# Kernel optimization log

Hardware: AMD Instinct MI355X
Metric: run time of the kernel (lower is better)

The kernel has to match this reference:

```python
import jax, jax.numpy as jnp
import numpy as np

A = 9
C = 80
TOPK = 1000            # topk_candidates
NMS_THRESH = 0.5
SCORE_THRESH = 0.05
DET_PER_IMG = 100      # detections_per_img
BBOX_XFORM_CLIP = float(np.log(1000.0 / 16.0))
CLASS_OFFSET = 4096.0  # > any clipped coordinate -> class-aware NMS trick


def setup_inputs() -> dict:
    key = jax.random.key(0)
    ks = jax.random.split(key, 4)
    B = 8
    levels = [(128, 128, 4096, 8), (64, 64, 2048, 16), (32, 32, 1024, 32)]  # H, W, K, stride
    inp = {}
    for i, (H, W, K, stride) in enumerate(levels):
        k1, k2, k3, k4, k5, k6, k7, k8 = jax.random.split(ks[i], 8)
        # plausible anchor boxes (x1, y1, x2, y2) with positive width/height
        cx = jax.random.uniform(k1, (B, H, W, A)) * (W * stride)
        cy = jax.random.uniform(k2, (B, H, W, A)) * (H * stride)
        w = 16.0 + jax.random.uniform(k3, (B, H, W, A)) * 112.0
        h = 16.0 + jax.random.uniform(k4, (B, H, W, A)) * 112.0
        anch = jnp.stack([cx - 0.5 * w, cy - 0.5 * h, cx + 0.5 * w, cy + 0.5 * h], axis=-1)
        # [B, H, W, A, 4] -> [B, 4A, H, W] (A groups of 4 along channel, matching permute(1,2,0) + reshape(-1,4))
        inp[f"anchors_{i}"] = jnp.transpose(anch.reshape(B, H, W, 4 * A), (0, 3, 1, 2)).astype(jnp.float32)
        coords = jnp.stack(
            [jax.random.randint(k5, (B, K), 0, H), jax.random.randint(k6, (B, K), 0, W)], axis=-1
        ).astype(jnp.int32)
        inp[f"coords_{i}"] = coords
        inp[f"score_logits_{i}"] = (jax.random.normal(k7, (B, K, A * C)) * 2.0 - 2.0).astype(jnp.float32)
        inp[f"regs_{i}"] = (jax.random.normal(k8, (B, K, A * 4)) * 0.2).astype(jnp.float32)
    inp["image_shapes"] = jnp.full((B, 2), 1024.0, dtype=jnp.float32)  # (h, w) per image
    return inp


def _decode(boxes, deltas, img_hw):
    # boxes, deltas: [N, 4] (x1, y1, x2, y2) / (dx, dy, dw, dh)
    x1, y1, x2, y2 = boxes[:, 0], boxes[:, 1], boxes[:, 2], boxes[:, 3]
    w = x2 - x1
    h = y2 - y1
    cx = x1 + 0.5 * w
    cy = y1 + 0.5 * h
    dx, dy = deltas[:, 0], deltas[:, 1]
    dw = jnp.minimum(deltas[:, 2], BBOX_XFORM_CLIP)
    dh = jnp.minimum(deltas[:, 3], BBOX_XFORM_CLIP)
    pcx = dx * w + cx
    pcy = dy * h + cy
    pw = jnp.exp(dw) * w
    ph = jnp.exp(dh) * h
    ih, iw = img_hw[0], img_hw[1]
    nx1 = jnp.clip(pcx - 0.5 * pw, 0.0, iw)
    ny1 = jnp.clip(pcy - 0.5 * ph, 0.0, ih)
    nx2 = jnp.clip(pcx + 0.5 * pw, 0.0, iw)
    ny2 = jnp.clip(pcy + 0.5 * ph, 0.0, ih)
    return jnp.stack([nx1, ny1, nx2, ny2], axis=-1)


def _level(anchor_map, coords, logits, regs, img_hw):
    # anchor_map: [4A, H, W]; coords: [K, 2]; logits: [K, A*C]; regs: [K, A*4]
    bb = jnp.transpose(anchor_map, (1, 2, 0))[coords[:, 0], coords[:, 1]]  # [K, 4A]
    boxes = bb.reshape(-1, 4)            # [K*A, 4]
    deltas = regs.reshape(-1, 4)         # [K*A, 4]
    dec = _decode(boxes, deltas, img_hw)
    scores = jax.nn.sigmoid(logits.reshape(-1, C))  # [K*A, C]
    flat = scores.reshape(-1)                       # [K*A*C]
    k = min(TOPK, flat.shape[0])
    top_s, idx = jax.lax.top_k(flat, k)
    return dec[idx // C], top_s, (idx % C)


def _pairwise_iou(b):
    area = (b[:, 2] - b[:, 0]) * (b[:, 3] - b[:, 1])
    lt = jnp.maximum(b[:, None, :2], b[None, :, :2])
    rb = jnp.minimum(b[:, None, 2:], b[None, :, 2:])
    wh = jnp.clip(rb - lt, 0.0)
    inter = wh[..., 0] * wh[..., 1]
    return inter / (area[:, None] + area[None, :] - inter + 1e-9)


def _nms(boxes, scores, labels):
    # class-aware NMS with fixed-size output [DET_PER_IMG, 6]
    order = jnp.argsort(-scores)
    b = boxes[order]
    s = scores[order]
    l = labels[order]
    iou = _pairwise_iou(b + l.astype(b.dtype)[:, None] * CLASS_OFFSET)  # [N, N]
    N = s.shape[0]
    idxs = jnp.arange(N)
    valid = s > SCORE_THRESH

    def body(i, keep):
        sup = (iou[i] > NMS_THRESH) & (idxs > i) & keep[i]
        return keep & ~sup

    keep = jax.lax.fori_loop(0, N, body, valid)
    masked = jnp.where(keep, s, -1.0)
    top_s, top_i = jax.lax.top_k(masked, DET_PER_IMG)
    pad = top_s > 0.0
    out_b = jnp.where(pad[:, None], b[top_i], 0.0)
    out_l = jnp.where(pad, l[top_i], -1).astype(b.dtype)
    return jnp.concatenate([out_b, top_s[:, None], out_l[:, None]], axis=-1)  # [DET, 6]


def _per_image(a0, a1, a2, c0, c1, c2, s0, s1, s2, r0, r1, r2, hw):
    parts = [
        _level(a, c, sl, r, hw)
        for a, c, sl, r in zip((a0, a1, a2), (c0, c1, c2), (s0, s1, s2), (r0, r1, r2))
    ]
    boxes = jnp.concatenate([p[0] for p in parts], axis=0)
    scores = jnp.concatenate([p[1] for p in parts], axis=0)
    labels = jnp.concatenate([p[2] for p in parts], axis=0)
    return _nms(boxes, scores, labels)


def reference(anchors_0, anchors_1, anchors_2, coords_0, coords_1, coords_2,
              score_logits_0, score_logits_1, score_logits_2,
              regs_0, regs_1, regs_2, image_shapes):
    # returns [B, DET_PER_IMG, 6] = (x1, y1, x2, y2, score, label); padded rows have score -1, label -1
    return jax.vmap(_per_image)(
        anchors_0, anchors_1, anchors_2,
        coords_0, coords_1, coords_2,
        score_logits_0, score_logits_1, score_logits_2,
        regs_0, regs_1, regs_2, image_shapes,
    )
```

## Files before the change

### kernel.cpp

```cpp
#include <hip/hip_runtime.h>

typedef unsigned long long u64;
typedef unsigned int u32;

#define NIMG 8
#define NLVL 3
#define TOPKN 1000
#define NC3 3000
#define DETS 100
#define PRETH 3.0f
#define NBINS 3072
#define LCAP 2048
#define MROWS 256
#define NW 47
#define NWP 48
#define CAP 32768
#define GPAD 16

#define NBLK0 5760
#define NBLK1 2880
#define NBLK2 1440
#define NBLKTOT 10080

__device__ __forceinline__ u32 fmap(float f) {
  u32 b = __float_as_uint(f);
  return (b & 0x80000000u) ? ~b : (b | 0x80000000u);
}
__device__ __forceinline__ float funmap(u32 u) {
  u32 b = (u & 0x80000000u) ? (u & 0x7FFFFFFFu) : ~u;
  return __uint_as_float(b);
}

__global__ __launch_bounds__(256) void k_prefilter(
    const float* __restrict__ lg0, const float* __restrict__ lg1,
    const float* __restrict__ lg2, u64* __restrict__ dense,
    u32* __restrict__ gcnt) {
  __shared__ int s_wcnt[4];
  __shared__ u32 s_base;
  const int tid = threadIdx.x, wave = tid >> 6, lane = tid & 63;
  int blk = blockIdx.x;
  const float* lg; int imgElems, lblk, lvl;
  if (blk < NBLK0)              { lg = lg0; imgElems = 2949120; lblk = blk; lvl = 0; }
  else if (blk < NBLK0 + NBLK1) { lg = lg1; imgElems = 1474560; lblk = blk - NBLK0; lvl = 1; }
  else                          { lg = lg2; imgElems = 737280;  lblk = blk - NBLK0 - NBLK1; lvl = 2; }
  int ce = lblk * 4096 + wave * 1024;
  int img = ce / imgElems;
  int flatBase = ce - img * imgElems;
  const float* src = lg + (size_t)img * imgElems;
  const int dst = img * NLVL + lvl;
  u64 lmask = (1ull << lane) - 1ull;
  float va[16];
#pragma unroll
  for (int r = 0; r < 4; ++r) {
    const float4 v = *(const float4*)(src + flatBase + r * 256 + lane * 4);
    va[r * 4 + 0] = v.x; va[r * 4 + 1] = v.y;
    va[r * 4 + 2] = v.z; va[r * 4 + 3] = v.w;
  }
  int total = 0;
#pragma unroll
  for (int u = 0; u < 16; ++u) total += __popcll(__ballot(va[u] > PRETH));
  if (lane == 0) s_wcnt[wave] = total;
  __syncthreads();
  if (tid == 0) {
    u32 bt = (u32)(s_wcnt[0] + s_wcnt[1] + s_wcnt[2] + s_wcnt[3]);
    s_base = bt ? atomicAdd(&gcnt[dst * GPAD], bt) : 0u;
  }
  __syncthreads();
  u32 base = s_base;
  for (int w2 = 0; w2 < wave; ++w2) base += (u32)s_wcnt[w2];
  u64* db = dense + (size_t)dst * CAP;
  int off = 0;
#pragma unroll
  for (int u = 0; u < 16; ++u) {
    bool p = va[u] > PRETH;
    u64 m = __ballot(p);
    if (p) {
      int idx = flatBase + (u >> 2) * 256 + lane * 4 + (u & 3);
      u32 fm = fmap(va[u]);
      u32 pos = base + (u32)(off + __popcll(m & lmask));
      if (pos < CAP) db[pos] = ((u64)fm << 32) | (u64)(~(u32)idx);
    }
    off += __popcll(m);
  }
}

__global__ __launch_bounds__(1024) void k_select(
    const u64* __restrict__ dense, const u32* __restrict__ gcnt,
    u64* __restrict__ topk) {
  __shared__ u32 hist[NBINS];
  __shared__ u64 lk[LCAP];
  __shared__ u32 wsum[16], wpre[16];
  __shared__ int sT, sM;
  const int bi = blockIdx.x;
  const int tid = threadIdx.x, wave = tid >> 6, lane = tid & 63;

  const u64 SAFE = ((u64)0x3E5FFFFFu << 32) | 0xFFFFFFFFull;
  if (tid < TOPKN) topk[(size_t)bi * TOPKN + tid] = SAFE;
  for (int i = tid; i < NBINS; i += 1024) hist[i] = 0;
  if (tid == 0) { sM = 0; sT = 0; }
  __syncthreads();

  u32 N = gcnt[bi * GPAD]; if (N > CAP) N = CAP;
  const u64* src = dense + (size_t)bi * CAP;
  for (u32 i = tid; i < N; i += 1024) {
    u32 bin = ((u32)(src[i] >> 32) - 0xC0000000u) >> 13;
    if (bin > NBINS - 1) bin = NBINS - 1;
    atomicAdd(&hist[bin], 1u);
  }
  __syncthreads();

  const int h0 = NBINS - 1 - tid * 3;
  u32 a0 = hist[h0], a1 = hist[h0 - 1], a2 = hist[h0 - 2];
  u32 s = a0 + a1 + a2;
  u32 inc = s;
#pragma unroll
  for (int d = 1; d < 64; d <<= 1) {
    u32 t = (u32)__shfl_up((int)inc, d);
    if (lane >= d) inc += t;
  }
  if (lane == 63) wsum[wave] = inc;
  __syncthreads();
  if (tid < 16) {
    u32 w = wsum[tid];
    u32 wi = w;
#pragma unroll
    for (int d = 1; d < 16; d <<= 1) {
      u32 t = (u32)__shfl_up((int)wi, d);
      if (tid >= d) wi += t;
    }
    wpre[tid] = wi - w;
  }
  __syncthreads();
  u32 excl = wpre[wave] + (inc - s);
  if (excl < TOPKN && excl + s >= TOPKN) {
    u32 acc = excl + a0;
    int T;
    if (acc >= TOPKN) T = h0;
    else { acc += a1; T = (acc >= TOPKN) ? h0 - 1 : h0 - 2; }
    sT = T;
  }
  __syncthreads();
  const int T = sT;

  for (u32 i = tid; i < N; i += 1024) {
    u64 key = src[i];
    u32 bin = ((u32)(key >> 32) - 0xC0000000u) >> 13;
    if (bin > NBINS - 1) bin = NBINS - 1;
    if ((int)bin >= T) {
      int q = atomicAdd(&sM, 1);
      if (q < LCAP) lk[q] = key;
    }
  }
  __syncthreads();
  int M = sM; if (M > LCAP) M = LCAP;
  u64 k0 = 0, k1 = 0;
  const bool have0 = tid < M, have1 = tid + 1024 < M;
  if (have0) k0 = lk[tid];
  if (have1) k1 = lk[tid + 1024];
  int r0 = 0, r1 = 0;
  for (int j = 0; j < M; ++j) {
    u64 kj = lk[j];
    r0 += (kj > k0);
    r1 += (kj > k1);
  }
  if (have0 && r0 < TOPKN) topk[(size_t)bi * TOPKN + r0] = k0;
  if (have1 && r1 < TOPKN) topk[(size_t)bi * TOPKN + r1] = k1;
}

__global__ __launch_bounds__(1024) void k_build(
    const u64* __restrict__ topk,
    const float* __restrict__ an0, const float* __restrict__ an1, const float* __restrict__ an2,
    const int* __restrict__ co0, const int* __restrict__ co1, const int* __restrict__ co2,
    const float* __restrict__ rg0, const float* __restrict__ rg1, const float* __restrict__ rg2,
    const float* __restrict__ ishape,
    float4* __restrict__ sbox, float* __restrict__ sscore, int* __restrict__ slabel) {
  __shared__ u64 keys[NC3];
  const int b = blockIdx.x, tid = threadIdx.x;
  const double ih = (double)ishape[b * 2 + 0];
  const double iw = (double)ishape[b * 2 + 1];
  const double CLIPV = 4.1351665567423563;
  float4 mb[3]; float ms[3]; int ml[3]; u64 mk[3]; bool mv[3];
  for (int q = 0; q < 3; ++q) {
    int c = tid + q * 1024;
    mv[q] = (c < NC3);
    mk[q] = 0ull;
    if (!mv[q]) continue;
    int l = c / 1000, pos = c - l * 1000;
    u64 key = topk[(size_t)(b * NLVL + l) * TOPKN + pos];
    u32 hi = (u32)(key >> 32);
    u32 flat = ~((u32)key);
    float logit = funmap(hi);
    int cls = (int)(flat % 80u);
    int bidx = (int)(flat / 80u);
    int k = bidx / 9, a = bidx - k * 9;
    const float* an; const int* co; const float* rg; int K, H, W;
    if (l == 0)      { an = an0; co = co0; rg = rg0; K = 4096; H = 128; W = 128; }
    else if (l == 1) { an = an1; co = co1; rg = rg1; K = 2048; H = 64;  W = 64;  }
    else             { an = an2; co = co2; rg = rg2; K = 1024; H = 32;  W = 32;  }
    if (k >= K) k = K - 1;
    int y = co[(b * K + k) * 2 + 0], x = co[(b * K + k) * 2 + 1];
    int HW = H * W;
    const float* ap = an + (size_t)(b * 36 + a * 4) * HW + y * W + x;
    double x1 = (double)ap[0], y1 = (double)ap[HW];
    double x2 = (double)ap[2 * HW], y2 = (double)ap[3 * HW];
    const float* rp = rg + (size_t)(b * K + k) * 36 + a * 4;
    double dx = (double)rp[0], dy = (double)rp[1];
    double dw = fmin((double)rp[2], CLIPV), dh = fmin((double)rp[3], CLIPV);
    double w = x2 - x1, h = y2 - y1;
    double cx = x1 + 0.5 * w, cy = y1 + 0.5 * h;
    double pcx = dx * w + cx, pcy = dy * h + cy;
    double pw = exp(dw) * w, ph = exp(dh) * h;
    double nx1 = fmin(fmax(pcx - 0.5 * pw, 0.0), iw);
    double ny1 = fmin(fmax(pcy - 0.5 * ph, 0.0), ih);
    double nx2 = fmin(fmax(pcx + 0.5 * pw, 0.0), iw);
    double ny2 = fmin(fmax(pcy + 0.5 * ph, 0.0), ih);
    mb[q] = make_float4((float)nx1, (float)ny1, (float)nx2, (float)ny2);
    ms[q] = (float)(1.0 / (1.0 + exp(-(double)logit)));
    ml[q] = cls;
    mk[q] = ((u64)hi << 32) | (u64)(~(u32)c);
    keys[c] = mk[q];
  }
  __syncthreads();
  for (int q = 0; q < 3; ++q) {
    if (!mv[q]) continue;
    int c = tid + q * 1024;
    int l = c / 1000, pos = c - l * 1000;
    int rank = pos;
    u64 key = mk[q];
#pragma unroll
    for (int m = 0; m < 3; ++m) {
      if (m == l) continue;
      int lo = 0, hi2 = 1000, base = m * 1000;
      while (lo < hi2) {
        int mid = (lo + hi2) >> 1;
        if (keys[base + mid] > key) lo = mid + 1; else hi2 = mid;
      }
      rank += lo;
    }
    sbox[(size_t)b * NC3 + rank] = mb[q];
    sscore[(size_t)b * NC3 + rank] = ms[q];
    slabel[(size_t)b * NC3 + rank] = ml[q];
  }
}

__global__ __launch_bounds__(256) void k_mask(
    const float4* __restrict__ sbox, const int* __restrict__ slabel,
    u64* __restrict__ mask) {
  __shared__ float4 qb[NC3];
  __shared__ float ar[NC3];
  const int img = blockIdx.x >> 4;
  const int r0 = (blockIdx.x & 15) * 16;
  const int tid = threadIdx.x, wave = tid >> 6, lane = tid & 63;
  for (int i = tid; i < NC3; i += 256) {
    float4 bx = sbox[(size_t)img * NC3 + i];
    float off = (float)slabel[(size_t)img * NC3 + i] * 4096.0f;
    float4 q = make_float4(bx.x + off, bx.y + off, bx.z + off, bx.w + off);
    qb[i] = q;
    ar[i] = (q.z - q.x) * (q.w - q.y);
  }
  __syncthreads();
  u64* mbase = mask + (size_t)img * MROWS * NWP;
  for (int q = 0; q < 4; ++q) {
    int i = r0 + wave * 4 + q;
    float4 bi = qb[i];
    float ai = ar[i];
    for (int w = 0; w < NW; ++w) {
      int j = w * 64 + lane;
      bool pred = false;
      if (j > i && j < NC3) {
        float4 bj = qb[j];
        float ltx = fmaxf(bi.x, bj.x), lty = fmaxf(bi.y, bj.y);
        float rbx = fminf(bi.z, bj.z), rby = fminf(bi.w, bj.w);
        float wx = fmaxf(rbx - ltx, 0.f), wy = fmaxf(rby - lty, 0.f);
        float inter = wx * wy;
        float denom = ((ai + ar[j]) - inter) + 1e-9f;
        pred = (inter / denom) > 0.5f;
      }
      u64 m = __ballot(pred);
      if (lane == 0) mbase[(size_t)i * NWP + w] = m;
    }
  }
}

__global__ __launch_bounds__(64) void k_serial(
    const float4* __restrict__ sbox, const float* __restrict__ sscore,
    const int* __restrict__ slabel, const u64* __restrict__ mask,
    float* __restrict__ out) {
  __shared__ int keptIdx[DETS];
  const int img = blockIdx.x, lane = threadIdx.x;
  const float* sc = sscore + (size_t)img * NC3;
  u64 mykeep = 0;
  for (int w = 0; w < NW; ++w) {
    int j = w * 64 + lane;
    float s = (j < NC3) ? sc[j] : -1.f;
    u64 m = __ballot(s > 0.05f);
    if (lane == w) mykeep = m;
  }
  const u64* mbase = mask + (size_t)img * MROWS * NWP;
  u64 pend[4];
  for (int d = 0; d < 4; ++d)
    pend[d] = (lane < NW) ? mbase[(size_t)d * NWP + lane] : 0ull;
  int cnt = 0;
  for (int i = 0; i < NC3; ++i) {
    u64 row = pend[i & 3];
    int nxt = i + 4;
    if (nxt < MROWS) pend[i & 3] = (lane < NW) ? mbase[(size_t)nxt * NWP + lane] : 0ull;
    int w = i >> 6;
    u64 kw = __shfl(mykeep, w);
    if ((kw >> (i & 63)) & 1ull) {
      if (lane == 0) keptIdx[cnt] = i;
      cnt++;
      if (cnt == DETS) break;
      if (i < MROWS) {
        mykeep &= ~row;
      } else {
        float4 bx = sbox[(size_t)img * NC3 + i];
        float off = (float)slabel[(size_t)img * NC3 + i] * 4096.0f;
        float bix = bx.x + off, biy = bx.y + off;
        float biz = bx.z + off, biw = bx.w + off;
        float ai = (biz - bix) * (biw - biy);
        for (int w2 = 0; w2 < NW; ++w2) {
          int j = w2 * 64 + lane;
          bool pred = false;
          if (j > i && j < NC3) {
            float4 bj = sbox[(size_t)img * NC3 + j];
            float o2 = (float)slabel[(size_t)img * NC3 + j] * 4096.0f;
            float jx = bj.x + o2, jy = bj.y + o2;
            float jz = bj.z + o2, jw = bj.w + o2;
            float aj = (jz - jx) * (jw - jy);
            float ltx = fmaxf(bix, jx), lty = fmaxf(biy, jy);
            float rbx = fminf(biz, jz), rby = fminf(biw, jw);
            float wx = fmaxf(rbx - ltx, 0.f), wy = fmaxf(rby - lty, 0.f);
            float inter = wx * wy;
            float denom = ((ai + aj) - inter) + 1e-9f;
            pred = (inter / denom) > 0.5f;
          }
          u64 m = __ballot(pred);
          if (lane == w2) mykeep &= ~m;
        }
      }
    }
  }
  __syncthreads();
  for (int s = lane; s < DETS; s += 64) {
    float* o = out + ((size_t)img * DETS + s) * 6;
    if (s < cnt) {
      int i = keptIdx[s];
      float4 bx = sbox[(size_t)img * NC3 + i];
      o[0] = bx.x; o[1] = bx.y; o[2] = bx.z; o[3] = bx.w;
      o[4] = sc[i];
      o[5] = (float)slabel[(size_t)img * NC3 + i];
    } else {
      o[0] = 0.f; o[1] = 0.f; o[2] = 0.f; o[3] = 0.f;
      o[4] = -1.0f; o[5] = -1.0f;
    }
  }
}

extern "C" void kernel_launch(void* const* d_in, const int* in_sizes, int n_in,
                              void* d_out, int out_size, void* d_ws, size_t ws_size,
                              hipStream_t stream) {
  int ia0, ic0, is0, ir0, ia1, ic1, is1, ir1, ia2, ic2, is2, ir2, ihw;
  if (in_sizes[1] == 8 * 4096 * 2) {
    ia0 = 0; ic0 = 1; is0 = 2; ir0 = 3;
    ia1 = 4; ic1 = 5; is1 = 6; ir1 = 7;
    ia2 = 8; ic2 = 9; is2 = 10; ir2 = 11; ihw = 12;
  } else {
    ia0 = 0; ia1 = 1; ia2 = 2;
    ic0 = 3; ic1 = 4; ic2 = 5;
    is0 = 6; is1 = 7; is2 = 8;
    ir0 = 9; ir1 = 10; ir2 = 11; ihw = 12;
  }

  u32* gcnt = (u32*)d_ws;
  u64* dense = (u64*)((char*)d_ws + 2048);
  u64* topk = dense + (size_t)NIMG * NLVL * CAP;
  float4* sboxp = (float4*)(topk + NIMG * NLVL * TOPKN);
  float* sscore = (float*)(sboxp + NIMG * NC3);
  int* slabel = (int*)(sscore + NIMG * NC3);
  u64* maskp = (u64*)(slabel + NIMG * NC3);
  float* out = (float*)d_out;

  hipMemsetAsync(d_ws, 0, 2048, stream);

  k_prefilter<<<NBLKTOT, 256, 0, stream>>>(
      (const float*)d_in[is0], (const float*)d_in[is1], (const float*)d_in[is2],
      dense, gcnt);
  k_select<<<NIMG * NLVL, 1024, 0, stream>>>(dense, gcnt, topk);
  k_build<<<NIMG, 1024, 0, stream>>>(topk,
      (const float*)d_in[ia0], (const float*)d_in[ia1], (const float*)d_in[ia2],
      (const int*)d_in[ic0], (const int*)d_in[ic1], (const int*)d_in[ic2],
      (const float*)d_in[ir0], (const float*)d_in[ir1], (const float*)d_in[ir2],
      (const float*)d_in[ihw],
      sboxp, sscore, slabel);
  k_mask<<<NIMG * 16, 256, 0, stream>>>(sboxp, slabel, maskp);
  k_serial<<<NIMG, 64, 0, stream>>>(sboxp, sscore, slabel, maskp, out);
}
```

Before: 415.5 us.

## Shard prefilter atomic counters per wave and stage NMS mask rows in LDS

The prefilter now has each wave reserve output slots with its own atomic on one of 32 sub-bucket counters per image-level. This removes the two block-wide barriers and the single hot atomic per image-level. k_select walks the 32 sub-buckets per wave instead of one dense list. Separately, k_serial runs with 256 threads to cooperatively stage the first 128 mask rows and all scores into LDS before the single-wave serial NMS loop. The risks are per-sub-bucket overflow (1536 slots each, which could drop candidates under skewed inputs) and a larger memset.

```diff
diff --git a/kernel.cpp b/kernel.cpp
--- a/kernel.cpp
+++ b/kernel.cpp
@@ -12,9 +12,11 @@
 #define NBINS 3072
 #define LCAP 2048
 #define MROWS 256
+#define MLDS 128
 #define NW 47
 #define NWP 48
-#define CAP 32768
+#define NSUB 32
+#define SUBCAP 1536
 #define GPAD 16
 
 #define NBLK0 5760
@@ -35,8 +37,6 @@
     const float* __restrict__ lg0, const float* __restrict__ lg1,
     const float* __restrict__ lg2, u64* __restrict__ dense,
     u32* __restrict__ gcnt) {
-  __shared__ int s_wcnt[4];
-  __shared__ u32 s_base;
   const int tid = threadIdx.x, wave = tid >> 6, lane = tid & 63;
   int blk = blockIdx.x;
   const float* lg; int imgElems, lblk, lvl;
@@ -48,6 +48,7 @@
   int flatBase = ce - img * imgElems;
   const float* src = lg + (size_t)img * imgElems;
   const int dst = img * NLVL + lvl;
+  const int sub = (lblk * 4 + wave) & (NSUB - 1);
   u64 lmask = (1ull << lane) - 1ull;
   float va[16];
 #pragma unroll
@@ -56,29 +57,26 @@
     va[r * 4 + 0] = v.x; va[r * 4 + 1] = v.y;
     va[r * 4 + 2] = v.z; va[r * 4 + 3] = v.w;
   }
+  u64 bm[16];
   int total = 0;
 #pragma unroll
-  for (int u = 0; u < 16; ++u) total += __popcll(__ballot(va[u] > PRETH));
-  if (lane == 0) s_wcnt[wave] = total;
-  __syncthreads();
-  if (tid == 0) {
-    u32 bt = (u32)(s_wcnt[0] + s_wcnt[1] + s_wcnt[2] + s_wcnt[3]);
-    s_base = bt ? atomicAdd(&gcnt[dst * GPAD], bt) : 0u;
-  }
-  __syncthreads();
-  u32 base = s_base;
-  for (int w2 = 0; w2 < wave; ++w2) base += (u32)s_wcnt[w2];
-  u64* db = dense + (size_t)dst * CAP;
+  for (int u = 0; u < 16; ++u) {
+    bm[u] = __ballot(va[u] > PRETH);
+    total += __popcll(bm[u]);
+  }
+  u32 base = 0;
+  if (lane == 0 && total)
+    base = atomicAdd(&gcnt[(dst * NSUB + sub) * GPAD], (u32)total);
+  base = (u32)__shfl((int)base, 0);
+  u64* db = dense + ((size_t)dst * NSUB + sub) * SUBCAP;
   int off = 0;
 #pragma unroll
   for (int u = 0; u < 16; ++u) {
-    bool p = va[u] > PRETH;
-    u64 m = __ballot(p);
-    if (p) {
+    u64 m = bm[u];
+    if ((m >> lane) & 1ull) {
       int idx = flatBase + (u >> 2) * 256 + lane * 4 + (u & 3);
-      u32 fm = fmap(va[u]);
       u32 pos = base + (u32)(off + __popcll(m & lmask));
-      if (pos < CAP) db[pos] = ((u64)fm << 32) | (u64)(~(u32)idx);
+      if (pos < SUBCAP) db[pos] = ((u64)fmap(va[u]) << 32) | (u64)(~(u32)idx);
     }
     off += __popcll(m);
   }
@@ -90,6 +88,7 @@
   __shared__ u32 hist[NBINS];
   __shared__ u64 lk[LCAP];
   __shared__ u32 wsum[16], wpre[16];
+  __shared__ u32 scnt[NSUB];
   __shared__ int sT, sM;
   const int bi = blockIdx.x;
   const int tid = threadIdx.x, wave = tid >> 6, lane = tid & 63;
@@ -97,15 +96,22 @@
   const u64 SAFE = ((u64)0x3E5FFFFFu << 32) | 0xFFFFFFFFull;
   if (tid < TOPKN) topk[(size_t)bi * TOPKN + tid] = SAFE;
   for (int i = tid; i < NBINS; i += 1024) hist[i] = 0;
+  if (tid < NSUB) {
+    u32 c = gcnt[(bi * NSUB + tid) * GPAD];
+    scnt[tid] = c > SUBCAP ? SUBCAP : c;
+  }
   if (tid == 0) { sM = 0; sT = 0; }
   __syncthreads();
 
-  u32 N = gcnt[bi * GPAD]; if (N > CAP) N = CAP;
-  const u64* src = dense + (size_t)bi * CAP;
-  for (u32 i = tid; i < N; i += 1024) {
-    u32 bin = ((u32)(src[i] >> 32) - 0xC0000000u) >> 13;
-    if (bin > NBINS - 1) bin = NBINS - 1;
-    atomicAdd(&hist[bin], 1u);
+  const u64* src = dense + (size_t)bi * NSUB * SUBCAP;
+  for (int s = wave; s < NSUB; s += 16) {
+    u32 c = scnt[s];
+    const u64* sp = src + (size_t)s * SUBCAP;
+    for (u32 i = lane; i < c; i += 64) {
+      u32 bin = ((u32)(sp[i] >> 32) - 0xC0000000u) >> 13;
+      if (bin > NBINS - 1) bin = NBINS - 1;
+      atomicAdd(&hist[bin], 1u);
+    }
   }
   __syncthreads();
 
@@ -142,13 +148,17 @@
   __syncthreads();
   const int T = sT;
 
-  for (u32 i = tid; i < N; i += 1024) {
-    u64 key = src[i];
-    u32 bin = ((u32)(key >> 32) - 0xC0000000u) >> 13;
-    if (bin > NBINS - 1) bin = NBINS - 1;
-    if ((int)bin >= T) {
-      int q = atomicAdd(&sM, 1);
-      if (q < LCAP) lk[q] = key;
+  for (int s2 = wave; s2 < NSUB; s2 += 16) {
+    u32 c = scnt[s2];
+    const u64* sp = src + (size_t)s2 * SUBCAP;
+    for (u32 i = lane; i < c; i += 64) {
+      u64 key = sp[i];
+      u32 bin = ((u32)(key >> 32) - 0xC0000000u) >> 13;
+      if (bin > NBINS - 1) bin = NBINS - 1;
+      if ((int)bin >= T) {
+        int q = atomicAdd(&sM, 1);
+        if (q < LCAP) lk[q] = key;
+      }
     }
   }
   __syncthreads();
@@ -282,73 +292,87 @@
   }
 }
 
-__global__ __launch_bounds__(64) void k_serial(
+__global__ __launch_bounds__(256) void k_serial(
     const float4* __restrict__ sbox, const float* __restrict__ sscore,
     const int* __restrict__ slabel, const u64* __restrict__ mask,
     float* __restrict__ out) {
+  __shared__ u64 sm_mask[MLDS * NWP];
+  __shared__ float sm_sc[NC3];
   __shared__ int keptIdx[DETS];
-  const int img = blockIdx.x, lane = threadIdx.x;
+  __shared__ int s_cnt;
+  const int img = blockIdx.x, tid = threadIdx.x, wave = tid >> 6, lane = tid & 63;
+  const u64* mbase = mask + (size_t)img * MROWS * NWP;
   const float* sc = sscore + (size_t)img * NC3;
-  u64 mykeep = 0;
-  for (int w = 0; w < NW; ++w) {
-    int j = w * 64 + lane;
-    float s = (j < NC3) ? sc[j] : -1.f;
-    u64 m = __ballot(s > 0.05f);
-    if (lane == w) mykeep = m;
-  }
-  const u64* mbase = mask + (size_t)img * MROWS * NWP;
-  u64 pend[4];
-  for (int d = 0; d < 4; ++d)
-    pend[d] = (lane < NW) ? mbase[(size_t)d * NWP + lane] : 0ull;
-  int cnt = 0;
-  for (int i = 0; i < NC3; ++i) {
-    u64 row = pend[i & 3];
-    int nxt = i + 4;
-    if (nxt < MROWS) pend[i & 3] = (lane < NW) ? mbase[(size_t)nxt * NWP + lane] : 0ull;
-    int w = i >> 6;
-    u64 kw = __shfl(mykeep, w);
-    if ((kw >> (i & 63)) & 1ull) {
-      if (lane == 0) keptIdx[cnt] = i;
-      cnt++;
-      if (cnt == DETS) break;
-      if (i < MROWS) {
-        mykeep &= ~row;
-      } else {
-        float4 bx = sbox[(size_t)img * NC3 + i];
-        float off = (float)slabel[(size_t)img * NC3 + i] * 4096.0f;
-        float bix = bx.x + off, biy = bx.y + off;
-        float biz = bx.z + off, biw = bx.w + off;
-        float ai = (biz - bix) * (biw - biy);
-        for (int w2 = 0; w2 < NW; ++w2) {
-          int j = w2 * 64 + lane;
-          bool pred = false;
-          if (j > i && j < NC3) {
-            float4 bj = sbox[(size_t)img * NC3 + j];
-            float o2 = (float)slabel[(size_t)img * NC3 + j] * 4096.0f;
-            float jx = bj.x + o2, jy = bj.y + o2;
-            float jz = bj.z + o2, jw = bj.w + o2;
-            float aj = (jz - jx) * (jw - jy);
-            float ltx = fmaxf(bix, jx), lty = fmaxf(biy, jy);
-            float rbx = fminf(biz, jz), rby = fminf(biw, jw);
-            float wx = fmaxf(rbx - ltx, 0.f), wy = fmaxf(rby - lty, 0.f);
-            float inter = wx * wy;
-            float denom = ((ai + aj) - inter) + 1e-9f;
-            pred = (inter / denom) > 0.5f;
+  for (int i = tid; i < MLDS * NWP; i += 256) sm_mask[i] = mbase[i];
+  for (int i = tid; i < NC3; i += 256) sm_sc[i] = sc[i];
+  __syncthreads();
+  if (wave == 0) {
+    u64 mykeep = 0;
+    for (int w = 0; w < NW; ++w) {
+      int j = w * 64 + lane;
+      float s = (j < NC3) ? sm_sc[j] : -1.f;
+      u64 m = __ballot(s > 0.05f);
+      if (lane == w) mykeep = m;
+    }
+    u64 pend[4];
+    for (int d = 0; d < 4; ++d)
+      pend[d] = (lane < NW) ? sm_mask[d * NWP + lane] : 0ull;
+    int cnt = 0;
+    for (int i = 0; i < NC3; ++i) {
+      u64 row = pend[i & 3];
+      int nxt = i + 4;
+      if (nxt < MROWS)
+        pend[i & 3] = (lane < NW)
+            ? ((nxt < MLDS) ? sm_mask[nxt * NWP + lane]
+                            : mbase[(size_t)nxt * NWP + lane])
+            : 0ull;
+      int w = i >> 6;
+      u64 kw = __shfl(mykeep, w);
+      if ((kw >> (i & 63)) & 1ull) {
+        if (lane == 0) keptIdx[cnt] = i;
+        cnt++;
+        if (cnt == DETS) break;
+        if (i < MROWS) {
+          mykeep &= ~row;
+        } else {
+          float4 bx = sbox[(size_t)img * NC3 + i];
+          float off = (float)slabel[(size_t)img * NC3 + i] * 4096.0f;
+          float bix = bx.x + off, biy = bx.y + off;
+          float biz = bx.z + off, biw = bx.w + off;
+          float ai = (biz - bix) * (biw - biy);
+          for (int w2 = 0; w2 < NW; ++w2) {
+            int j = w2 * 64 + lane;
+            bool pred = false;
+            if (j > i && j < NC3) {
+              float4 bj = sbox[(size_t)img * NC3 + j];
+              float o2 = (float)slabel[(size_t)img * NC3 + j] * 4096.0f;
+              float jx = bj.x + o2, jy = bj.y + o2;
+              float jz = bj.z + o2, jw = bj.w + o2;
+              float aj = (jz - jx) * (jw - jy);
+              float ltx = fmaxf(bix, jx), lty = fmaxf(biy, jy);
+              float rbx = fminf(biz, jz), rby = fminf(biw, jw);
+              float wx = fmaxf(rbx - ltx, 0.f), wy = fmaxf(rby - lty, 0.f);
+              float inter = wx * wy;
+              float denom = ((ai + aj) - inter) + 1e-9f;
+              pred = (inter / denom) > 0.5f;
+            }
+            u64 m = __ballot(pred);
+            if (lane == w2) mykeep &= ~m;
           }
-          u64 m = __ballot(pred);
-          if (lane == w2) mykeep &= ~m;
         }
       }
     }
-  }
-  __syncthreads();
-  for (int s = lane; s < DETS; s += 64) {
+    if (lane == 0) s_cnt = cnt;
+  }
+  __syncthreads();
+  const int cnt = s_cnt;
+  for (int s = tid; s < DETS; s += 256) {
     float* o = out + ((size_t)img * DETS + s) * 6;
     if (s < cnt) {
       int i = keptIdx[s];
       float4 bx = sbox[(size_t)img * NC3 + i];
       o[0] = bx.x; o[1] = bx.y; o[2] = bx.z; o[3] = bx.w;
-      o[4] = sc[i];
+      o[4] = sm_sc[i];
       o[5] = (float)slabel[(size_t)img * NC3 + i];
     } else {
       o[0] = 0.f; o[1] = 0.f; o[2] = 0.f; o[3] = 0.f;
@@ -373,15 +397,15 @@
   }
 
   u32* gcnt = (u32*)d_ws;
-  u64* dense = (u64*)((char*)d_ws + 2048);
-  u64* topk = dense + (size_t)NIMG * NLVL * CAP;
+  u64* dense = (u64*)((char*)d_ws + 49152);
+  u64* topk = dense + (size_t)NIMG * NLVL * NSUB * SUBCAP;
   float4* sboxp = (float4*)(topk + NIMG * NLVL * TOPKN);
   float* sscore = (float*)(sboxp + NIMG * NC3);
   int* slabel = (int*)(sscore + NIMG * NC3);
   u64* maskp = (u64*)(slabel + NIMG * NC3);
   float* out = (float*)d_out;
 
-  hipMemsetAsync(d_ws, 0, 2048, stream);
+  hipMemsetAsync(d_ws, 0, 49152, stream);
 
   k_prefilter<<<NBLKTOT, 256, 0, stream>>>(
       (const float*)d_in[is0], (const float*)d_in[is1], (const float*)d_in[is2],
@@ -394,5 +418,5 @@
       (const float*)d_in[ihw],
       sboxp, sscore, slabel);
   k_mask<<<NIMG * 16, 256, 0, stream>>>(sboxp, slabel, maskp);
-  k_serial<<<NIMG, 64, 0, stream>>>(sboxp, sscore, slabel, maskp, out);
-}
+  k_serial<<<NIMG, 256, 0, stream>>>(sboxp, sscore, slabel, maskp, out);
+}
```

Measured after the change: 390.9 us. 1.06x faster.
